# Optimization experiments

Measured on AMD Instinct MI355X. Metric: run time of the kernel, lower is better.

The kernel has to match this reference:

```python
import jax, jax.numpy as jnp
import numpy as np

B = 4
CPD = 64            # control_plane_dim
RES = 64            # n_resonances
N_SAMPLES = 131072
CONTROL_RATE = 256
N_FRAMES = N_SAMPLES // CONTROL_RATE  # 512
FILTER_SIZE = 2048
HID = 16            # hypernetwork hidden
BASE_RESONANCE = 0.5
MAX_RESONANCE = 0.9999


def _sequential_damping(forces, damping):
    # forces, damping: (b, cpd, T); out[0]=f[0]; out[i]=(f[i]+out[i-1])*d[i]
    f_t = jnp.moveaxis(forces, -1, 0)   # (T, b, cpd)
    d_t = jnp.moveaxis(damping, -1, 0)  # (T, b, cpd)
    first = jnp.zeros((f_t.shape[0],), dtype=bool).at[0].set(True)

    def step(carry, xs):
        f, d, fst = xs
        out = jnp.where(fst, f, (f + carry) * d)
        return out, out

    _, ys = jax.lax.scan(step, jnp.zeros_like(f_t[0]), (f_t, d_t, first))
    return jnp.moveaxis(ys, 0, -1)


def _interp_linear(x, out_size):
    # F.interpolate(mode='linear', align_corners=False) along last axis
    n = x.shape[-1]
    pos = (jnp.arange(out_size, dtype=jnp.float32) + 0.5) * (n / out_size) - 0.5
    pos = jnp.clip(pos, 0.0, n - 1)
    i0 = jnp.floor(pos).astype(jnp.int32)
    i1 = jnp.minimum(i0 + 1, n - 1)
    frac = (pos - i0).astype(x.dtype)
    return x[..., i0] * (1.0 - frac) + x[..., i1] * frac


def _fft_convolve(a, b):
    # pad both to 2N, multiply spectra, keep first N (linear convolution)
    n = a.shape[-1]
    pa = jnp.pad(a, [(0, 0)] * (a.ndim - 1) + [(0, n)])
    pb = jnp.pad(b, [(0, 0)] * (b.ndim - 1) + [(0, n)])
    spec = jnp.fft.rfft(pa, axis=-1) * jnp.fft.rfft(pb, axis=-1)
    return jnp.fft.irfft(spec, axis=-1)[..., :n]


def setup_inputs() -> dict:
    key = jax.random.key(0)
    ks = jax.random.split(key, 9)
    forces = jax.random.normal(ks[0], (B, CPD, N_FRAMES), jnp.float32) * 0.1
    damping_modifier = jax.random.normal(ks[1], (B, CPD, N_FRAMES), jnp.float32) * 0.001
    noise = jax.random.uniform(ks[2], (B, RES, N_SAMPLES), jnp.float32, -0.01, 0.01)
    damping_param = jnp.zeros((1, CPD, 1), jnp.float32)
    routing = jax.random.uniform(ks[3], (1, 1, CPD, RES), jnp.float32, -0.01, 0.01)
    W1 = jax.random.normal(ks[4], (CPD, HID), jnp.float32) / jnp.sqrt(jnp.float32(CPD))
    b1 = jnp.zeros((HID,), jnp.float32)
    W2 = jax.random.normal(ks[5], (HID, CPD * RES), jnp.float32) / jnp.sqrt(jnp.float32(HID))
    b2 = jnp.zeros((CPD * RES,), jnp.float32)
    filters = jax.random.uniform(ks[6], (1, RES, FILTER_SIZE), jnp.float32, -0.01, 0.01)
    to_control = jax.random.uniform(ks[7], (RES, CPD), jnp.float32, -0.01, 0.01)
    return dict(forces=forces, damping_modifier=damping_modifier, noise=noise,
                damping_param=damping_param, routing=routing,
                W1=W1, b1=b1, W2=W2, b2=b2,
                filters=filters, to_control=to_control)


def reference(forces, damping_modifier, noise, damping_param, routing,
              W1, b1, W2, b2, filters, to_control):
    batch = forces.shape[0]
    # Damping module
    damping = BASE_RESONANCE + jax.nn.sigmoid(damping_param) * (MAX_RESONANCE - BASE_RESONANCE)
    damping = jnp.broadcast_to(damping, (1, CPD, N_FRAMES))
    damping = jnp.clip(damping - jnp.abs(damping_modifier), 0.0, 1.0)  # (b,cpd,T)
    damped = _sequential_damping(forces, damping)                       # (b,cpd,T)

    # HyperNetworkLayer: per-frame routing weight modifier
    x = jnp.swapaxes(damped, 1, 2)                      # (b, T, cpd)
    h = jax.nn.leaky_relu(x @ W1 + b1, negative_slope=0.2)
    w = (h @ W2 + b2).reshape(batch, N_FRAMES, CPD, RES)
    w = w + routing                                      # (b, T, cpd, res)

    routed = jnp.einsum('abc,acbd->adc', damped, w)      # (b, res, T)
    to_ctrl = jnp.einsum('brf,rc->bcf', routed, to_control)  # (b, cpd, T)

    upsampled = _interp_linear(routed, N_SAMPLES)        # (b, res, N)
    energy = upsampled * noise
    filt = jnp.pad(filters, ((0, 0), (0, 0), (0, N_SAMPLES - FILTER_SIZE)))
    with_resonance = _fft_convolve(energy, filt)         # (b, res, N)
    return to_ctrl, with_resonance
```

## Files before the change

### kernel.cpp

```cpp
#include <hip/hip_runtime.h>
#include <cstdint>

#define BATCH 4
#define CPD 64
#define RES 64
#define NS 131072
#define NF 512
#define FS 2048
#define HID 16

typedef _Float16 __attribute__((ext_vector_type(8))) f16x8;
typedef float __attribute__((ext_vector_type(16))) f32x16;

typedef union { uint4 u; f16x8 v; } Frag;

__global__ __launch_bounds__(256) void k_scan(const float* __restrict__ forces,
                                              const float* __restrict__ dmod,
                                              const float* __restrict__ dparam,
                                              float* __restrict__ damped_t) {
  __shared__ float f_lds[64][129];
  __shared__ float d_lds[64][129];
  const int b = blockIdx.x;
  const int tid = threadIdx.x;
  float dbase = 0.f, carry = 0.f;
  if (tid < 64) {
    float dp = dparam[tid];
    dbase = 0.5f + (0.9999f - 0.5f) / (1.f + expf(-dp));
  }
  for (int ch = 0; ch < 4; ++ch) {
    const int t0 = ch * 128;
    __syncthreads();
    for (int idx = tid; idx < 64 * 128; idx += 256) {
      int c = idx >> 7, tl = idx & 127;
      f_lds[c][tl] = forces[(b * CPD + c) * NF + t0 + tl];
      d_lds[c][tl] = dmod[(b * CPD + c) * NF + t0 + tl];
    }
    __syncthreads();
    if (tid < 64) {
      const int c = tid;
      for (int tl = 0; tl < 128; ++tl) {
        float d = dbase - fabsf(d_lds[c][tl]);
        d = fminf(fmaxf(d, 0.f), 1.f);
        float f = f_lds[c][tl];
        float out = (ch == 0 && tl == 0) ? f : (f + carry) * d;
        carry = out;
        damped_t[(b * NF + t0 + tl) * CPD + c] = out;
      }
    }
  }
}

__global__ __launch_bounds__(256) void k_hyper(const float* __restrict__ damped_t,
                                               const float* __restrict__ routing,
                                               const float* __restrict__ W1,
                                               const float* __restrict__ b1,
                                               const float* __restrict__ W2,
                                               const float* __restrict__ b2,
                                               const float* __restrict__ to_control,
                                               float* __restrict__ routed,
                                               float* __restrict__ to_ctrl) {
  __shared__ float xs[4][64];
  __shared__ float hs[4][16];
  __shared__ float rs[4][64];
  const int blk = blockIdx.x;
  const int b = blk >> 7;
  const int t0 = (blk & 127) * 4;
  const int lt = threadIdx.x >> 6;
  const int d = threadIdx.x & 63;
  const int t = t0 + lt;

  xs[lt][d] = damped_t[(b * NF + t) * CPD + d];
  __syncthreads();
  if (d < HID) {
    float a = b1[d];
    for (int c = 0; c < CPD; ++c) a = fmaf(xs[lt][c], W1[c * HID + d], a);
    hs[lt][d] = a > 0.f ? a : 0.2f * a;
  }
  __syncthreads();
  float hreg[HID];
#pragma unroll
  for (int j = 0; j < HID; ++j) hreg[j] = hs[lt][j];

  float acc = 0.f;
  for (int c = 0; c < CPD; ++c) {
    float w = routing[c * RES + d] + b2[c * RES + d];
    const float* w2p = W2 + c * RES + d;
#pragma unroll
    for (int j = 0; j < HID; ++j) w = fmaf(hreg[j], w2p[j * (CPD * RES)], w);
    acc = fmaf(xs[lt][c], w, acc);
  }
  routed[(b * RES + d) * NF + t] = acc;
  rs[lt][d] = acc;
  __syncthreads();
  float tc = 0.f;
  for (int q = 0; q < RES; ++q) tc = fmaf(rs[lt][q], to_control[q * CPD + d], tc);
  to_ctrl[(b * CPD + d) * NF + t] = tc;
}

__global__ __launch_bounds__(256) void k_zero(float* __restrict__ reso) {
  const int chan = blockIdx.x;
  const size_t base = (size_t)chan * NS;
  for (int i = threadIdx.x; i < 8192; i += 256) {
    int y;
    if (i < 32) y = i;
    else if (i < 32 + 7168) {
      int s = 1 + ((i - 32) >> 10);
      y = 16384 * s - 992 + ((i - 32) & 1023);
    } else {
      y = 130080 + (i - 7200);
    }
    reso[base + y] = 0.f;
  }
}

#define SPAN 16384
#define ER_GRAN 2312
#define ER_N 18432
#define FC_COPIES 8
#define FC_STRIDE 267
#define SMEM_BYTES (ER_GRAN * 16 + FC_COPIES * FC_STRIDE * 16)

__global__ __launch_bounds__(512, 4) void k_conv(const float* __restrict__ routed,
                                                 const float* __restrict__ noise,
                                                 const float* __restrict__ filters,
                                                 float* __restrict__ outp) {
  __shared__ __align__(16) unsigned char smem[SMEM_BYTES];
  unsigned char* erb = smem;
  unsigned char* fcb = smem + ER_GRAN * 16;

  const int tid = threadIdx.x;
  const int seg = blockIdx.x & 7;
  const int r = (blockIdx.x >> 3) & 63;
  const int b = blockIdx.x >> 9;
  const int NB = seg * SPAN;
  const int E0 = NB + SPAN + 32;
  const int chan = b * RES + r;
  const float* rp = routed + chan * NF;
  const float* npz = noise + (size_t)chan * NS;

  {
    unsigned* f32p = (unsigned*)fcb;
    const float* fr = filters + r * FS;
    for (int idx = tid; idx < FC_COPIES * FC_STRIDE * 4; idx += 512) {
      int c = idx / (FC_STRIDE * 4);
      int d = idx - c * (FC_STRIDE * 4);
      int t0 = 2 * d + c - 32;
      float f0 = (t0 >= 0 && t0 < FS) ? fr[t0] : 0.f;
      float f1 = (t0 + 1 >= 0 && t0 + 1 < FS) ? fr[t0 + 1] : 0.f;
      union { _Float16 h[2]; unsigned u; } P;
      P.h[0] = (_Float16)f0;
      P.h[1] = (_Float16)f1;
      f32p[idx] = P.u;
    }
  }

  {
    unsigned* er32 = (unsigned*)erb;
    for (int x2 = tid; x2 < ER_N / 2; x2 += 512) {
      int x = 2 * x2;
      union { _Float16 h[2]; unsigned u; } P;
#pragma unroll
      for (int k = 0; k < 2; ++k) {
        int n = E0 - x - k;
        float e = 0.f;
        if (n >= 0 && n < NS) {
          float pos = ((float)n + 0.5f) * (1.f / 256.f) - 0.5f;
          pos = fminf(fmaxf(pos, 0.f), 511.f);
          float fi = floorf(pos);
          int i0 = (int)fi;
          int i1 = min(i0 + 1, 511);
          float fr = pos - fi;
          float u = rp[i0] * (1.f - fr) + rp[i1] * fr;
          e = u * npz[n];
        }
        P.h[k] = (_Float16)(e * 1024.f);
      }
      int g = x >> 3;
      int sig = g ^ ((g >> 3) & 7);
      er32[sig * 4 + ((x & 7) >> 1)] = P.u;
    }
  }
  __syncthreads();

  const int w = tid >> 6;
  const int l = tid & 63;
  const int row = l & 31;
  const int h = l >> 5;

  const int gaA = 2048 - 256 * w + 4 * row + h;
  const int gaB = gaA - 128;
  const int qcb = (row & 7) * FC_STRIDE + (row >> 3) + h;

  f32x16 p00, p01, p10, p11;
#pragma unroll
  for (int i = 0; i < 16; ++i) { p00[i] = 0.f; p01[i] = 0.f; p10[i] = 0.f; p11[i] = 0.f; }

#define LOADA(DST, GB, SG_)                                                   \
  { int g = (GB) + 2 * (SG_); int ab = (g ^ ((g >> 3) & 7)) << 4;             \
    DST.u = *(const uint4*)(erb + ab); }
#define LOADBF(DST, SG_, J_)                                                  \
  { int gb = qcb + 2 * (SG_) + 128 * (J_);                                    \
    DST.u = *(const uint4*)(fcb + (gb << 4)); }

  for (int sg = 0; sg < 2; ++sg) {
    Frag B0, A0, A1;
    LOADBF(B0, sg, 0)
    LOADA(A0, gaA, sg) LOADA(A1, gaB, sg)
    p00 = __builtin_amdgcn_mfma_f32_32x32x16_f16(A0.v, B0.v, p00, 0, 0, 0);
    p10 = __builtin_amdgcn_mfma_f32_32x32x16_f16(A1.v, B0.v, p10, 0, 0, 0);
  }
  for (int sg = 2; sg < 66; ++sg) {
    Frag B0, B1, A0, A1;
    LOADBF(B0, sg, 0) LOADBF(B1, sg, 1)
    LOADA(A0, gaA, sg) LOADA(A1, gaB, sg)
    p00 = __builtin_amdgcn_mfma_f32_32x32x16_f16(A0.v, B0.v, p00, 0, 0, 0);
    p01 = __builtin_amdgcn_mfma_f32_32x32x16_f16(A0.v, B1.v, p01, 0, 0, 0);
    p10 = __builtin_amdgcn_mfma_f32_32x32x16_f16(A1.v, B0.v, p10, 0, 0, 0);
    p11 = __builtin_amdgcn_mfma_f32_32x32x16_f16(A1.v, B1.v, p11, 0, 0, 0);
  }

  if (seg == 7 && w == 7) {
    f32x16 ax;
#pragma unroll
    for (int i = 0; i < 16; ++i) ax[i] = 0.f;
    const int ge = 4 * row + h;
    for (int sg = 0; sg < 66; ++sg) {
      Frag Bx, Ax;
      LOADBF(Bx, sg, 0)
      LOADA(Ax, ge, sg)
      ax = __builtin_amdgcn_mfma_f32_32x32x16_f16(Ax.v, Bx.v, ax, 0, 0, 0);
    }
#pragma unroll
    for (int i = 0; i < 16; ++i) p11[i] += ax[i];
  }
#undef LOADA
#undef LOADBF

  float* cbase = outp + (size_t)chan * NS;
  const float scale = 1.f / 1024.f;

  {
    float* po = cbase + NB + 1024 * (2 * w + 1);
#pragma unroll
    for (int rg = 0; rg < 16; ++rg) {
      int crow = (rg & 3) + 8 * (rg >> 2) + 4 * h;
      po[row - 32 * crow] = (p10[rg] + p01[rg]) * scale;
    }
  }

  __syncthreads();
  float* scr = (float*)smem;
#pragma unroll
  for (int rg = 0; rg < 16; ++rg) scr[w * 1024 + rg * 64 + l] = p11[rg];
  __syncthreads();

  if (w >= 1) {
    float* po = cbase + NB + 1024 * (2 * w);
#pragma unroll
    for (int rg = 0; rg < 16; ++rg) {
      int crow = (rg & 3) + 8 * (rg >> 2) + 4 * h;
      po[row - 32 * crow] = (p00[rg] + scr[(w - 1) * 1024 + rg * 64 + l]) * scale;
    }
  } else {
#pragma unroll
    for (int rg = 0; rg < 16; ++rg) {
      int crow = (rg & 3) + 8 * (rg >> 2) + 4 * h;
      int y = NB + row - 32 * crow;
      if (y >= 0) atomicAdd(cbase + y, p00[rg] * scale);
    }
  }
  if (w == 7) {
#pragma unroll
    for (int rg = 0; rg < 16; ++rg) {
      int crow = (rg & 3) + 8 * (rg >> 2) + 4 * h;
      int y = NB + SPAN + row - 32 * crow;
      if (y < NS) atomicAdd(cbase + y, p11[rg] * scale);
    }
  }
}

extern "C" void kernel_launch(void* const* d_in, const int* in_sizes, int n_in,
                              void* d_out, int out_size, void* d_ws, size_t ws_size,
                              hipStream_t stream) {
  const float* forces     = (const float*)d_in[0];
  const float* dmod       = (const float*)d_in[1];
  const float* noise      = (const float*)d_in[2];
  const float* dparam     = (const float*)d_in[3];
  const float* routing    = (const float*)d_in[4];
  const float* W1         = (const float*)d_in[5];
  const float* b1         = (const float*)d_in[6];
  const float* W2         = (const float*)d_in[7];
  const float* b2         = (const float*)d_in[8];
  const float* filters    = (const float*)d_in[9];
  const float* to_control = (const float*)d_in[10];

  float* out = (float*)d_out;
  float* to_ctrl = out;
  float* reso = out + BATCH * CPD * NF;

  float* damped_t = (float*)d_ws;
  float* routed = damped_t + BATCH * NF * CPD;

  k_scan<<<BATCH, 256, 0, stream>>>(forces, dmod, dparam, damped_t);
  k_hyper<<<BATCH * NF / 4, 256, 0, stream>>>(damped_t, routing, W1, b1, W2, b2,
                                              to_control, routed, to_ctrl);
  k_zero<<<BATCH * RES, 256, 0, stream>>>(reso);
  k_conv<<<BATCH * RES * (NS / SPAN), 512, 0, stream>>>(routed, noise, filters, reso);
}
```

Before: 250.0 us.

## Precompute fp16 energy and filter layouts in separate kernels before convolution

Adds k_energy, which computes the upsampled energy (interpolated routing times noise) once per channel, writes it as reversed fp16 vectors to workspace, and k_filter, which writes the pre-swizzled fp16 filter copies. k_conv then only copies these precomputed buffers into shared memory. This removes the interpolation and filter repacking that each of the eight segment blocks per channel used to redo, including the overlapping halo regions. The cost is an extra roughly 68 MB workspace round trip and two more launches. It falls back to the old path when the workspace is too small.

After: 305.7 us. 22.3% more time.

```diff
diff --git a/kernel.cpp b/kernel.cpp
--- a/kernel.cpp
+++ b/kernel.cpp
@@ -118,12 +118,64 @@
 #define ER_N 18432
 #define FC_COPIES 8
 #define FC_STRIDE 267
+#define FGL_DW (FC_COPIES * FC_STRIDE * 4)
 #define SMEM_BYTES (ER_GRAN * 16 + FC_COPIES * FC_STRIDE * 16)
+#define GR_CH 16648
+
+__global__ __launch_bounds__(256) void k_energy(const float* __restrict__ routed,
+                                                const float* __restrict__ noise,
+                                                uint4* __restrict__ erev) {
+  const int idx = blockIdx.x * 256 + threadIdx.x;
+  const int chan = idx / GR_CH;
+  const int y8 = idx - chan * GR_CH;
+  const float* rp = routed + chan * NF;
+  const float* np = noise + (size_t)chan * NS;
+  const int n0 = 131128 - 8 * y8;
+  union { _Float16 h[8]; uint4 u; } P;
+#pragma unroll
+  for (int k = 0; k < 8; ++k) {
+    int n = n0 - k;
+    float e = 0.f;
+    if (n >= 0 && n < NS) {
+      float pos = ((float)n + 0.5f) * (1.f / 256.f) - 0.5f;
+      pos = fminf(fmaxf(pos, 0.f), 511.f);
+      float fi = floorf(pos);
+      int i0 = (int)fi;
+      int i1 = min(i0 + 1, 511);
+      float fr = pos - fi;
+      float u = rp[i0] * (1.f - fr) + rp[i1] * fr;
+      e = u * np[n];
+    }
+    P.h[k] = (_Float16)(e * 1024.f);
+  }
+  erev[idx] = P.u;
+}
+
+__global__ __launch_bounds__(256) void k_filter(const float* __restrict__ filters,
+                                                unsigned* __restrict__ fgl) {
+  const int r = blockIdx.x;
+  const float* fr = filters + r * FS;
+  unsigned* dst = fgl + r * FGL_DW;
+  for (int idx = threadIdx.x; idx < FGL_DW; idx += 256) {
+    int c = idx / (FC_STRIDE * 4);
+    int d = idx - c * (FC_STRIDE * 4);
+    int t0 = 2 * d + c - 32;
+    float f0 = (t0 >= 0 && t0 < FS) ? fr[t0] : 0.f;
+    float f1 = (t0 + 1 >= 0 && t0 + 1 < FS) ? fr[t0 + 1] : 0.f;
+    union { _Float16 h[2]; unsigned u; } P;
+    P.h[0] = (_Float16)f0;
+    P.h[1] = (_Float16)f1;
+    dst[idx] = P.u;
+  }
+}
 
 __global__ __launch_bounds__(512, 4) void k_conv(const float* __restrict__ routed,
                                                  const float* __restrict__ noise,
                                                  const float* __restrict__ filters,
-                                                 float* __restrict__ outp) {
+                                                 float* __restrict__ outp,
+                                                 const uint4* __restrict__ erev,
+                                                 const unsigned* __restrict__ fgl,
+                                                 int use_pre) {
   __shared__ __align__(16) unsigned char smem[SMEM_BYTES];
   unsigned char* erb = smem;
   unsigned char* fcb = smem + ER_GRAN * 16;
@@ -135,13 +187,21 @@
   const int NB = seg * SPAN;
   const int E0 = NB + SPAN + 32;
   const int chan = b * RES + r;
-  const float* rp = routed + chan * NF;
-  const float* npz = noise + (size_t)chan * NS;
-
-  {
+
+  if (use_pre) {
+    const int o8 = 16387 - (seg + 1) * 2048;
+    const uint4* ef = erev + (size_t)chan * GR_CH + o8;
+    uint4* er4 = (uint4*)erb;
+    for (int s = tid; s < 2304; s += 512) er4[s] = ef[s ^ ((s >> 3) & 7)];
+    const uint4* fg = (const uint4*)(fgl + r * FGL_DW);
+    uint4* fc4 = (uint4*)fcb;
+    for (int q = tid; q < FGL_DW / 4; q += 512) fc4[q] = fg[q];
+  } else {
+    const float* rp = routed + chan * NF;
+    const float* npz = noise + (size_t)chan * NS;
     unsigned* f32p = (unsigned*)fcb;
     const float* fr = filters + r * FS;
-    for (int idx = tid; idx < FC_COPIES * FC_STRIDE * 4; idx += 512) {
+    for (int idx = tid; idx < FGL_DW; idx += 512) {
       int c = idx / (FC_STRIDE * 4);
       int d = idx - c * (FC_STRIDE * 4);
       int t0 = 2 * d + c - 32;
@@ -152,9 +212,6 @@
       P.h[1] = (_Float16)f1;
       f32p[idx] = P.u;
     }
-  }
-
-  {
     unsigned* er32 = (unsigned*)erb;
     for (int x2 = tid; x2 < ER_N / 2; x2 += 512) {
       int x = 2 * x2;
@@ -169,8 +226,8 @@
           float fi = floorf(pos);
           int i0 = (int)fi;
           int i1 = min(i0 + 1, 511);
-          float fr = pos - fi;
-          float u = rp[i0] * (1.f - fr) + rp[i1] * fr;
+          float fr2 = pos - fi;
+          float u = rp[i0] * (1.f - fr2) + rp[i1] * fr2;
           e = u * npz[n];
         }
         P.h[k] = (_Float16)(e * 1024.f);
@@ -298,12 +355,22 @@
   float* to_ctrl = out;
   float* reso = out + BATCH * CPD * NF;
 
-  float* damped_t = (float*)d_ws;
-  float* routed = damped_t + BATCH * NF * CPD;
+  char* ws = (char*)d_ws;
+  float* damped_t = (float*)ws;
+  float* routed = (float*)(ws + (512 << 10));
+  unsigned* fgl = (unsigned*)(ws + (1 << 20));
+  uint4* erev = (uint4*)(ws + (4 << 20));
+  const size_t need = (size_t)(4 << 20) + (size_t)256 * GR_CH * 16;
+  const int use_pre = (ws_size >= need) ? 1 : 0;
 
   k_scan<<<BATCH, 256, 0, stream>>>(forces, dmod, dparam, damped_t);
   k_hyper<<<BATCH * NF / 4, 256, 0, stream>>>(damped_t, routing, W1, b1, W2, b2,
                                               to_control, routed, to_ctrl);
+  if (use_pre) {
+    k_filter<<<RES, 256, 0, stream>>>(filters, fgl);
+    k_energy<<<GR_CH, 256, 0, stream>>>(routed, noise, erev);
+  }
   k_zero<<<BATCH * RES, 256, 0, stream>>>(reso);
-  k_conv<<<BATCH * RES * (NS / SPAN), 512, 0, stream>>>(routed, noise, filters, reso);
-}
+  k_conv<<<BATCH * RES * (NS / SPAN), 512, 0, stream>>>(routed, noise, filters,
+                                                        reso, erev, fgl, use_pre);
+}
```

## Precompute fp16 filter layout once and vectorize energy staging in conv

Applied to the files above, without the earlier changes.

The fp16 filter conversion and layout that k_conv did inside each of its 2048 blocks now runs once per resonance in a new k_filter kernel writing to workspace, and k_conv copies it into LDS with 16-byte loads. The energy staging loop now handles 8 samples per thread using float4 noise loads, two interpolation anchor pairs and a single 16-byte swizzled LDS store, in place of scalar per-sample loads and 4-byte stores. This cuts redundant conversion work and the number of scalar global and LDS accesses in the conv prologue, at the cost of an extra kernel launch and a workspace round trip.

Result: faster. 224.1 us (-10.4%).

```diff
diff --git a/kernel.cpp b/kernel.cpp
--- a/kernel.cpp
+++ b/kernel.cpp
@@ -115,15 +115,33 @@
 
 #define SPAN 16384
 #define ER_GRAN 2312
-#define ER_N 18432
 #define FC_COPIES 8
 #define FC_STRIDE 267
+#define FGL_DW (FC_COPIES * FC_STRIDE * 4)
 #define SMEM_BYTES (ER_GRAN * 16 + FC_COPIES * FC_STRIDE * 16)
+
+__global__ __launch_bounds__(256) void k_filter(const float* __restrict__ filters,
+                                                unsigned* __restrict__ fgl) {
+  const int r = blockIdx.x;
+  const float* fr = filters + r * FS;
+  unsigned* dst = fgl + r * FGL_DW;
+  for (int idx = threadIdx.x; idx < FGL_DW; idx += 256) {
+    int c = idx / (FC_STRIDE * 4);
+    int d = idx - c * (FC_STRIDE * 4);
+    int t0 = 2 * d + c - 32;
+    float f0 = (t0 >= 0 && t0 < FS) ? fr[t0] : 0.f;
+    float f1 = (t0 + 1 >= 0 && t0 + 1 < FS) ? fr[t0 + 1] : 0.f;
+    union { _Float16 h[2]; unsigned u; } P;
+    P.h[0] = (_Float16)f0;
+    P.h[1] = (_Float16)f1;
+    dst[idx] = P.u;
+  }
+}
 
 __global__ __launch_bounds__(512, 4) void k_conv(const float* __restrict__ routed,
                                                  const float* __restrict__ noise,
-                                                 const float* __restrict__ filters,
-                                                 float* __restrict__ outp) {
+                                                 float* __restrict__ outp,
+                                                 const unsigned* __restrict__ fgl) {
   __shared__ __align__(16) unsigned char smem[SMEM_BYTES];
   unsigned char* erb = smem;
   unsigned char* fcb = smem + ER_GRAN * 16;
@@ -135,50 +153,58 @@
   const int NB = seg * SPAN;
   const int E0 = NB + SPAN + 32;
   const int chan = b * RES + r;
-  const float* rp = routed + chan * NF;
-  const float* npz = noise + (size_t)chan * NS;
 
   {
-    unsigned* f32p = (unsigned*)fcb;
-    const float* fr = filters + r * FS;
-    for (int idx = tid; idx < FC_COPIES * FC_STRIDE * 4; idx += 512) {
-      int c = idx / (FC_STRIDE * 4);
-      int d = idx - c * (FC_STRIDE * 4);
-      int t0 = 2 * d + c - 32;
-      float f0 = (t0 >= 0 && t0 < FS) ? fr[t0] : 0.f;
-      float f1 = (t0 + 1 >= 0 && t0 + 1 < FS) ? fr[t0 + 1] : 0.f;
-      union { _Float16 h[2]; unsigned u; } P;
-      P.h[0] = (_Float16)f0;
-      P.h[1] = (_Float16)f1;
-      f32p[idx] = P.u;
-    }
+    const uint4* fg = (const uint4*)(fgl + r * FGL_DW);
+    uint4* fc4 = (uint4*)fcb;
+#pragma unroll
+    for (int k = 0; k < 4; ++k) fc4[tid + 512 * k] = fg[tid + 512 * k];
+    if (tid < FGL_DW / 4 - 2048) fc4[2048 + tid] = fg[2048 + tid];
   }
 
   {
-    unsigned* er32 = (unsigned*)erb;
-    for (int x2 = tid; x2 < ER_N / 2; x2 += 512) {
-      int x = 2 * x2;
-      union { _Float16 h[2]; unsigned u; } P;
-#pragma unroll
-      for (int k = 0; k < 2; ++k) {
-        int n = E0 - x - k;
-        float e = 0.f;
-        if (n >= 0 && n < NS) {
-          float pos = ((float)n + 0.5f) * (1.f / 256.f) - 0.5f;
-          pos = fminf(fmaxf(pos, 0.f), 511.f);
-          float fi = floorf(pos);
-          int i0 = (int)fi;
-          int i1 = min(i0 + 1, 511);
-          float fr = pos - fi;
-          float u = rp[i0] * (1.f - fr) + rp[i1] * fr;
-          e = u * npz[n];
-        }
-        P.h[k] = (_Float16)(e * 1024.f);
-      }
-      int g = x >> 3;
-      int sig = g ^ ((g >> 3) & 7);
-      er32[sig * 4 + ((x & 7) >> 1)] = P.u;
-    }
+    const float* rp = routed + chan * NF;
+    const float* npz = noise + (size_t)chan * NS;
+    const int n0base = E0 - 18431;
+
+#define STAGEG(T_)                                                            \
+    {                                                                         \
+      const int t_ = (T_);                                                    \
+      const int n0 = n0base + 8 * t_;                                         \
+      const int g = 2303 - t_;                                                \
+      const int nc = min(max(n0, 0), NS - 8);                                 \
+      const float4 na = *(const float4*)(npz + nc);                           \
+      const float4 nb = *(const float4*)(npz + nc + 4);                       \
+      float pos0 = fminf(fmaxf(fmaf((float)n0 + 0.5f, 1.f / 256.f, -0.5f), 0.f), 511.f); \
+      float pos7 = fminf(fmaxf(fmaf((float)n0 + 7.5f, 1.f / 256.f, -0.5f), 0.f), 511.f); \
+      const int ia = min((int)pos0, 510);                                     \
+      const int ib = min((int)pos7, 510);                                     \
+      const float c0 = rp[ia], c1 = rp[ia + 1];                               \
+      const float c2 = rp[ib], c3 = rp[ib + 1];                               \
+      const float iaf = (float)ia;                                            \
+      const float nv[8] = {na.x, na.y, na.z, na.w, nb.x, nb.y, nb.z, nb.w};   \
+      union { _Float16 h[8]; uint4 u; } O;                                    \
+      _Pragma("unroll")                                                       \
+      for (int k = 0; k < 8; ++k) {                                           \
+        const int n = n0 + k;                                                 \
+        float pos = fminf(fmaxf(fmaf((float)n + 0.5f, 1.f / 256.f, -0.5f), 0.f), 511.f); \
+        float i0f = fminf(floorf(pos), 510.f);                                \
+        float fr = pos - i0f;                                                 \
+        bool sel = i0f > iaf;                                                 \
+        float lo = sel ? c2 : c0;                                             \
+        float hi = sel ? c3 : c1;                                             \
+        float u = fmaf(fr, hi - lo, lo);                                      \
+        float e = (n >= 0 && n < NS) ? u * nv[k] * 1024.f : 0.f;              \
+        O.h[7 - k] = (_Float16)e;                                             \
+      }                                                                       \
+      const int gs = g ^ ((g >> 3) & 7);                                      \
+      *(uint4*)(erb + (gs << 4)) = O.u;                                       \
+    }
+
+#pragma unroll
+    for (int k = 0; k < 4; ++k) STAGEG(tid + 512 * k)
+    if (tid < 256) STAGEG(2048 + tid)
+#undef STAGEG
   }
   __syncthreads();
 
@@ -298,12 +324,15 @@
   float* to_ctrl = out;
   float* reso = out + BATCH * CPD * NF;
 
-  float* damped_t = (float*)d_ws;
-  float* routed = damped_t + BATCH * NF * CPD;
+  char* ws = (char*)d_ws;
+  float* damped_t = (float*)ws;
+  float* routed = (float*)(ws + (512 << 10));
+  unsigned* fgl = (unsigned*)(ws + (1 << 20));
 
   k_scan<<<BATCH, 256, 0, stream>>>(forces, dmod, dparam, damped_t);
   k_hyper<<<BATCH * NF / 4, 256, 0, stream>>>(damped_t, routing, W1, b1, W2, b2,
                                               to_control, routed, to_ctrl);
+  k_filter<<<RES, 256, 0, stream>>>(filters, fgl);
   k_zero<<<BATCH * RES, 256, 0, stream>>>(reso);
-  k_conv<<<BATCH * RES * (NS / SPAN), 512, 0, stream>>>(routed, noise, filters, reso);
-}
+  k_conv<<<BATCH * RES * (NS / SPAN), 512, 0, stream>>>(routed, noise, reso, fgl);
+}
```
